# Performance work log

Hardware: AMD Instinct MI355X
Metric: run time of the kernel (lower is better)

## Reference

```python
import jax, jax.numpy as jnp
import numpy as np

N = 50000      # nodes
E = 800000     # edges
F_IN = 128     # in_channels
H = 128        # hidden_channels
C = 10         # num_classes
G = 512        # graphs in batch
EPS = 1e-5     # batchnorm eps


def setup_inputs() -> dict:
    key = jax.random.key(0)
    ks = jax.random.split(key, 18)
    s = 0.05
    return {
        "x": jax.random.normal(ks[0], (N, F_IN), jnp.float32),
        "edge_index": jax.random.randint(ks[1], (2, E), 0, N, dtype=jnp.int32),
        "batch": jnp.sort(jax.random.randint(ks[2], (N,), 0, G, dtype=jnp.int32)),
        "W1": jax.random.normal(ks[3], (F_IN, H), jnp.float32) * s,
        "b1": jnp.zeros((H,), jnp.float32),
        "gamma1": jnp.ones((H,), jnp.float32),
        "beta1": jnp.zeros((H,), jnp.float32),
        "mean1": jax.random.normal(ks[4], (H,), jnp.float32) * 0.1,
        "var1": jax.random.uniform(ks[5], (H,), jnp.float32, 0.5, 1.5),
        "W2": jax.random.normal(ks[6], (H, H), jnp.float32) * s,
        "b2": jnp.zeros((H,), jnp.float32),
        "gamma2": jnp.ones((H,), jnp.float32),
        "beta2": jnp.zeros((H,), jnp.float32),
        "mean2": jax.random.normal(ks[7], (H,), jnp.float32) * 0.1,
        "var2": jax.random.uniform(ks[8], (H,), jnp.float32, 0.5, 1.5),
        "Wlin": jax.random.normal(ks[9], (H, C), jnp.float32) * s,
        "blin": jnp.zeros((C,), jnp.float32),
    }


def _gcn_conv(x, W, b, src, dst):
    # GCNConv with add_self_loops=True, symmetric normalization.
    h = x @ W                                             # [N, H]
    deg = jax.ops.segment_sum(jnp.ones((E,), h.dtype), dst, num_segments=N) + 1.0
    dis = jax.lax.rsqrt(deg)                              # deg^{-1/2}, [N]
    norm = dis[src] * dis[dst]                            # [E]
    agg = jax.ops.segment_sum(h[src] * norm[:, None], dst, num_segments=N)
    agg = agg + h * (dis * dis)[:, None]                  # self-loop term
    return agg + b


def _bn_eval(x, gamma, beta, mean, var):
    return gamma * (x - mean) * jax.lax.rsqrt(var + EPS) + beta


def reference(x, edge_index, batch, W1, b1, gamma1, beta1, mean1, var1,
              W2, b2, gamma2, beta2, mean2, var2, Wlin, blin):
    src, dst = edge_index[0], edge_index[1]
    h = _gcn_conv(x, W1, b1, src, dst)
    h = jax.nn.relu(_bn_eval(h, gamma1, beta1, mean1, var1))
    # dropout: identity in eval mode
    h = _gcn_conv(h, W2, b2, src, dst)
    h = jax.nn.relu(_bn_eval(h, gamma2, beta2, mean2, var2))
    # global_mean_pool over graph ids
    sums = jax.ops.segment_sum(h, batch, num_segments=G)          # [G, H]
    cnts = jax.ops.segment_sum(jnp.ones((N,), h.dtype), batch, num_segments=G)
    pooled = sums / jnp.maximum(cnts, 1.0)[:, None]
    return pooled @ Wlin + blin                                   # [G, C]
```

## Files before the change

kernel.cpp:

```cpp
#include <hip/hip_runtime.h>
#include <hip/hip_bf16.h>
#include <hip/hip_fp16.h>

#define N_NODES 50000
#define N_EDGES 800000
#define HDIM 128
#define NGRAPH 512
#define NCLS 10
#define BN_EPS 1e-5f
#define MAXDEG 64

typedef unsigned int   uint32;
typedef unsigned short u16;
typedef __attribute__((ext_vector_type(8))) _Float16 half8;
typedef __attribute__((ext_vector_type(4))) float f32x4;

__device__ inline u16 f2h(float f) {
    return __half_as_ushort(__float2half(f));
}
__device__ inline float2 h2f2(uint32 u) {
    __half2 h = *(__half2*)&u;
    return __half22float2(h);
}
__device__ inline uint32 packh2(float lo, float hi) {
    return (uint32)f2h(lo) | ((uint32)f2h(hi) << 16);
}

#define GEMM1_BLOCKS 1563
#define W2T_BLOCKS 8
#define FRONT_GRID (W2T_BLOCKS + 3 * GEMM1_BLOCKS)

__global__ __launch_bounds__(256) void front(const float* __restrict__ x,
                                             const float* __restrict__ W1,
                                             u16* __restrict__ bufA,
                                             const int* __restrict__ src,
                                             const int* __restrict__ dst,
                                             int* __restrict__ deg,
                                             u16* __restrict__ epad,
                                             const float* __restrict__ W2,
                                             u16* __restrict__ W2t)
{
    __shared__ float xs[32][36];
    __shared__ float ws[32][128];
    const int tid = threadIdx.x;
    int bid = blockIdx.x;

    if (bid < W2T_BLOCKS) {
        int t0 = bid * 256 + tid;
        for (int i = t0; i < HDIM * HDIM; i += W2T_BLOCKS * 256) {
            int k = i >> 7, n = i & 127;
            W2t[n * HDIM + k] = f2h(W2[i]);
        }
        return;
    }
    bid -= W2T_BLOCKS;
    const int grp = bid / 3, rem = bid % 3;

    if (rem != 0) {
        int e = (grp * 2 + (rem - 1)) * 256 + tid;
        if (e < N_EDGES) {
            int d   = dst[e];
            int pos = atomicAdd(&deg[d], 1);
            epad[d * MAXDEG + pos] = (u16)src[e];
        }
        return;
    }

    const int row0 = grp * 32;
    const int tx   = tid & 31;
    const int ty   = tid >> 5;

    float acc[4][4];
    #pragma unroll
    for (int i = 0; i < 4; ++i)
        #pragma unroll
        for (int j = 0; j < 4; ++j) acc[i][j] = 0.f;

    const int lr = tid >> 3;
    const int lk = (tid & 7) << 2;
    const int wr = tid >> 5;
    const int wc = (tid & 31) << 2;

    for (int k0 = 0; k0 < 128; k0 += 32) {
        float4 xv = make_float4(0.f, 0.f, 0.f, 0.f);
        int grow = row0 + lr;
        if (grow < N_NODES) xv = *(const float4*)(x + (size_t)grow * HDIM + k0 + lk);
        xs[lr][lk] = xv.x; xs[lr][lk + 1] = xv.y; xs[lr][lk + 2] = xv.z; xs[lr][lk + 3] = xv.w;
        #pragma unroll
        for (int i = 0; i < 4; ++i) {
            int kk = wr + i * 8;
            *(float4*)&ws[kk][wc] = *(const float4*)(W1 + (size_t)(k0 + kk) * HDIM + wc);
        }
        __syncthreads();
        #pragma unroll
        for (int kk = 0; kk < 32; kk += 4) {
            float4 wv[4];
            #pragma unroll
            for (int j = 0; j < 4; ++j) wv[j] = *(const float4*)&ws[kk + j][tx << 2];
            #pragma unroll
            for (int i = 0; i < 4; ++i) {
                float4 xr = *(const float4*)&xs[ty * 4 + i][kk];
                acc[i][0] += xr.x * wv[0].x; acc[i][1] += xr.x * wv[0].y;
                acc[i][2] += xr.x * wv[0].z; acc[i][3] += xr.x * wv[0].w;
                acc[i][0] += xr.y * wv[1].x; acc[i][1] += xr.y * wv[1].y;
                acc[i][2] += xr.y * wv[1].z; acc[i][3] += xr.y * wv[1].w;
                acc[i][0] += xr.z * wv[2].x; acc[i][1] += xr.z * wv[2].y;
                acc[i][2] += xr.z * wv[2].z; acc[i][3] += xr.z * wv[2].w;
                acc[i][0] += xr.w * wv[3].x; acc[i][1] += xr.w * wv[3].y;
                acc[i][2] += xr.w * wv[3].z; acc[i][3] += xr.w * wv[3].w;
            }
        }
        __syncthreads();
    }
    #pragma unroll
    for (int i = 0; i < 4; ++i) {
        int grow = row0 + ty * 4 + i;
        if (grow < N_NODES) {
            uint2 o;
            o.x = packh2(acc[i][0], acc[i][1]);
            o.y = packh2(acc[i][2], acc[i][3]);
            *(uint2*)(bufA + (size_t)grow * HDIM + (tx << 2)) = o;
        }
    }
}

#define BT_STRIDE 144
__global__ __launch_bounds__(256) void gemm2_mfma(const u16* __restrict__ A,
                                                  const u16* __restrict__ W2t,
                                                  u16* __restrict__ Y, int nrows)
{
    __shared__ u16 bt[HDIM * BT_STRIDE];
    const int tid = threadIdx.x;
    for (int i = tid; i < HDIM * HDIM / 8; i += 256) {
        int n  = i >> 4;
        int k8 = (i & 15) << 3;
        *(uint4*)&bt[n * BT_STRIDE + k8] = *(const uint4*)&W2t[n * HDIM + k8];
    }
    __syncthreads();

    const int wave = tid >> 6, lane = tid & 63;
    const int rowbase = blockIdx.x * 64 + wave * 16;
    if (rowbase >= nrows) return;
    const int n = lane & 15, q = lane >> 4;

    half8 a[4];
    const u16* arow = A + (size_t)(rowbase + n) * HDIM;
    #pragma unroll
    for (int kc = 0; kc < 4; ++kc)
        a[kc] = *(const half8*)(arow + kc * 32 + q * 8);

    #pragma unroll
    for (int t = 0; t < 8; ++t) {
        f32x4 acc = {0.f, 0.f, 0.f, 0.f};
        #pragma unroll
        for (int kc = 0; kc < 4; ++kc) {
            half8 b = *(const half8*)&bt[(t * 16 + n) * BT_STRIDE + kc * 32 + q * 8];
            acc = __builtin_amdgcn_mfma_f32_16x16x32_f16(a[kc], b, acc, 0, 0, 0);
        }
        #pragma unroll
        for (int r = 0; r < 4; ++r) {
            int grow = rowbase + q * 4 + r;
            Y[(size_t)grow * HDIM + t * 16 + n] = f2h(acc[r]);
        }
    }
}

__global__ __launch_bounds__(256) void gather_bn_relu(const u16* __restrict__ h,
                                                      const u16* __restrict__ epad,
                                                      const int* __restrict__ deg,
                                                      const float* __restrict__ b,
                                                      const float* __restrict__ gamma,
                                                      const float* __restrict__ beta,
                                                      const float* __restrict__ mean,
                                                      const float* __restrict__ var,
                                                      u16* __restrict__ out, int n)
{
    int node = blockIdx.x * 4 + (threadIdx.x >> 6);
    if (node >= n) return;
    const int lane = threadIdx.x & 63;
    const int q    = lane >> 4;
    const int ci   = (lane & 15) << 3;
    const int cnt_e = deg[node];
    const float dd  = rsqrtf((float)cnt_e + 1.0f);

    uint4 hv = *(const uint4*)(h + (size_t)node * HDIM + ci);

    int   s_all  = 0;
    float nm_all = 0.f;
    if (lane < cnt_e) {
        s_all  = epad[node * MAXDEG + lane];
        nm_all = rsqrtf((float)deg[s_all] + 1.0f) * dd;
    }

    float acc[8] = {0.f, 0.f, 0.f, 0.f, 0.f, 0.f, 0.f, 0.f};
    int j = q;
    for (; j + 4 < cnt_e; j += 8) {
        int   s0 = __shfl(s_all, j);     float nm0 = __shfl(nm_all, j);
        int   s1 = __shfl(s_all, j + 4); float nm1 = __shfl(nm_all, j + 4);
        uint4 v0 = *(const uint4*)(h + (size_t)s0 * HDIM + ci);
        uint4 v1 = *(const uint4*)(h + (size_t)s1 * HDIM + ci);
        float2 f0 = h2f2(v0.x), f1 = h2f2(v0.y), f2 = h2f2(v0.z), f3 = h2f2(v0.w);
        acc[0] += f0.x * nm0; acc[1] += f0.y * nm0;
        acc[2] += f1.x * nm0; acc[3] += f1.y * nm0;
        acc[4] += f2.x * nm0; acc[5] += f2.y * nm0;
        acc[6] += f3.x * nm0; acc[7] += f3.y * nm0;
        float2 g0 = h2f2(v1.x), g1 = h2f2(v1.y), g2 = h2f2(v1.z), g3 = h2f2(v1.w);
        acc[0] += g0.x * nm1; acc[1] += g0.y * nm1;
        acc[2] += g1.x * nm1; acc[3] += g1.y * nm1;
        acc[4] += g2.x * nm1; acc[5] += g2.y * nm1;
        acc[6] += g3.x * nm1; acc[7] += g3.y * nm1;
    }
    if (j < cnt_e) {
        int   s0 = __shfl(s_all, j); float nm0 = __shfl(nm_all, j);
        uint4 v0 = *(const uint4*)(h + (size_t)s0 * HDIM + ci);
        float2 f0 = h2f2(v0.x), f1 = h2f2(v0.y), f2 = h2f2(v0.z), f3 = h2f2(v0.w);
        acc[0] += f0.x * nm0; acc[1] += f0.y * nm0;
        acc[2] += f1.x * nm0; acc[3] += f1.y * nm0;
        acc[4] += f2.x * nm0; acc[5] += f2.y * nm0;
        acc[6] += f3.x * nm0; acc[7] += f3.y * nm0;
    }
    #pragma unroll
    for (int k = 0; k < 8; ++k) {
        acc[k] += __shfl_xor(acc[k], 16);
        acc[k] += __shfl_xor(acc[k], 32);
    }

    if (q == 0) {
        float2 g0 = h2f2(hv.x), g1 = h2f2(hv.y), g2 = h2f2(hv.z), g3 = h2f2(hv.w);
        float dd2 = dd * dd;
        float a[8] = {acc[0] + g0.x * dd2, acc[1] + g0.y * dd2,
                      acc[2] + g1.x * dd2, acc[3] + g1.y * dd2,
                      acc[4] + g2.x * dd2, acc[5] + g2.y * dd2,
                      acc[6] + g3.x * dd2, acc[7] + g3.y * dd2};
        float o[8];
        #pragma unroll
        for (int k = 0; k < 8; ++k) {
            int c = ci + k;
            float sc = gamma[c] * rsqrtf(var[c] + BN_EPS);
            float r  = (a[k] + b[c] - mean[c]) * sc + beta[c];
            o[k] = fmaxf(r, 0.f);
        }
        uint4 ov;
        ov.x = packh2(o[0], o[1]); ov.y = packh2(o[2], o[3]);
        ov.z = packh2(o[4], o[5]); ov.w = packh2(o[6], o[7]);
        *(uint4*)(out + (size_t)node * HDIM + ci) = ov;
    }
}

__global__ __launch_bounds__(128) void pool_sum(const u16* __restrict__ h,
                                                const int* __restrict__ batch,
                                                float* __restrict__ sums,
                                                float* __restrict__ cnt, int n)
{
    int c  = threadIdx.x;
    int n0 = blockIdx.x * 32;
    if (n0 >= n) return;
    int nend = min(n0 + 32, n);
    int curg = batch[n0];
    float acc = 0.f;
    int run = 0;
    for (int i = n0; i < nend; ++i) {
        int g   = batch[i];
        float v = __half2float(__ushort_as_half(h[(size_t)i * HDIM + c]));
        if (g != curg) {
            atomicAdd(&sums[(size_t)curg * HDIM + c], acc);
            if (c == 0) atomicAdd(&cnt[curg], (float)run);
            acc = 0.f; run = 0; curg = g;
        }
        acc += v; run++;
    }
    atomicAdd(&sums[(size_t)curg * HDIM + c], acc);
    if (c == 0) atomicAdd(&cnt[curg], (float)run);
}

__global__ __launch_bounds__(128) void final_lin(const float* __restrict__ sums,
                                                 const float* __restrict__ cnt,
                                                 const float* __restrict__ Wlin,
                                                 const float* __restrict__ blin,
                                                 float* __restrict__ out)
{
    __shared__ float red[NCLS][2];
    int g = blockIdx.x;
    int t = threadIdx.x;
    float ic = 1.f / fmaxf(cnt[g], 1.f);
    float v  = sums[(size_t)g * HDIM + t] * ic;
    float p[NCLS];
    #pragma unroll
    for (int c = 0; c < NCLS; ++c) p[c] = v * Wlin[t * NCLS + c];
    #pragma unroll
    for (int c = 0; c < NCLS; ++c) {
        float x = p[c];
        for (int off = 32; off > 0; off >>= 1) x += __shfl_down(x, off);
        if ((t & 63) == 0) red[c][t >> 6] = x;
    }
    __syncthreads();
    if (t < NCLS) out[g * NCLS + t] = red[t][0] + red[t][1] + blin[t];
}

extern "C" void kernel_launch(void* const* d_in, const int* in_sizes, int n_in,
                              void* d_out, int out_size, void* d_ws, size_t ws_size,
                              hipStream_t stream)
{
    const float* x     = (const float*)d_in[0];
    const int*   ei    = (const int*)d_in[1];
    const int*   srcp  = ei;
    const int*   dstp  = ei + N_EDGES;
    const int*   batch = (const int*)d_in[2];
    const float* W1    = (const float*)d_in[3];
    const float* b1    = (const float*)d_in[4];
    const float* g1    = (const float*)d_in[5];
    const float* be1   = (const float*)d_in[6];
    const float* m1    = (const float*)d_in[7];
    const float* v1    = (const float*)d_in[8];
    const float* W2    = (const float*)d_in[9];
    const float* b2    = (const float*)d_in[10];
    const float* g2    = (const float*)d_in[11];
    const float* be2   = (const float*)d_in[12];
    const float* m2    = (const float*)d_in[13];
    const float* v2    = (const float*)d_in[14];
    const float* Wlin  = (const float*)d_in[15];
    const float* blin  = (const float*)d_in[16];
    float*       out   = (float*)d_out;

    int*   deg  = (int*)d_ws;
    float* cnt  = (float*)(deg + N_NODES);
    float* sums = cnt + NGRAPH;
    u16*   bufA = (u16*)(sums + (size_t)NGRAPH * HDIM);
    u16*   bufB = bufA + (size_t)N_NODES * HDIM;
    u16*   epad = bufB + (size_t)N_NODES * HDIM;
    u16*   W2t  = epad + (size_t)N_NODES * MAXDEG;

    hipMemsetAsync(deg, 0,
                   (N_NODES + NGRAPH + (size_t)NGRAPH * HDIM) * sizeof(float), stream);

    front<<<FRONT_GRID, 256, 0, stream>>>(x, W1, bufA, srcp, dstp, deg, epad, W2, W2t);

    const int gather_blocks = (N_NODES + 3) / 4;

    gather_bn_relu<<<gather_blocks, 256, 0, stream>>>(bufA, epad, deg,
                                                      b1, g1, be1, m1, v1, bufB, N_NODES);
    gemm2_mfma<<<(N_NODES + 63) / 64, 256, 0, stream>>>(bufB, W2t, bufA, N_NODES);
    gather_bn_relu<<<gather_blocks, 256, 0, stream>>>(bufA, epad, deg,
                                                      b2, g2, be2, m2, v2, bufB, N_NODES);
    pool_sum<<<(N_NODES + 31) / 32, 128, 0, stream>>>(bufB, batch, sums, cnt, N_NODES);
    final_lin<<<NGRAPH, 128, 0, stream>>>(sums, cnt, Wlin, blin, out);
}
```

Measured before the change: 258.2 us.

## Compute first GCN GEMM with split-fp16 MFMA instead of fp32 SIMT

Replaces the fp32 shared-memory SIMT GEMM for x@W1 in the front kernel with MFMA 16x16x32 f16 instructions. Both x and W1 are split into hi and lo fp16 parts and combined with three MFMAs, to keep accuracy close to fp32. Each GEMM block now covers 64 rows, so the fused front grid is regrouped to four edge-bucketing blocks per GEMM block. Every block converts and transposes the full W1 into LDS using scalar stores, which adds per-block setup cost and may cause bank conflicts.

```diff
diff --git a/kernel.cpp b/kernel.cpp
--- a/kernel.cpp
+++ b/kernel.cpp
@@ -18,6 +18,9 @@
 __device__ inline u16 f2h(float f) {
     return __half_as_ushort(__float2half(f));
 }
+__device__ inline float h2f(u16 u) {
+    return __half2float(__ushort_as_half(u));
+}
 __device__ inline float2 h2f2(uint32 u) {
     __half2 h = *(__half2*)&u;
     return __half22float2(h);
@@ -26,9 +29,10 @@
     return (uint32)f2h(lo) | ((uint32)f2h(hi) << 16);
 }
 
-#define GEMM1_BLOCKS 1563
 #define W2T_BLOCKS 8
-#define FRONT_GRID (W2T_BLOCKS + 3 * GEMM1_BLOCKS)
+#define G1_BLOCKS 782
+#define FRONT_GRID (W2T_BLOCKS + 5 * G1_BLOCKS)
+#define BT_STRIDE 144
 
 __global__ __launch_bounds__(256) void front(const float* __restrict__ x,
                                              const float* __restrict__ W1,
@@ -40,8 +44,8 @@
                                              const float* __restrict__ W2,
                                              u16* __restrict__ W2t)
 {
-    __shared__ float xs[32][36];
-    __shared__ float ws[32][128];
+    __shared__ u16 bt_hi[HDIM * BT_STRIDE];
+    __shared__ u16 bt_lo[HDIM * BT_STRIDE];
     const int tid = threadIdx.x;
     int bid = blockIdx.x;
 
@@ -54,10 +58,10 @@
         return;
     }
     bid -= W2T_BLOCKS;
-    const int grp = bid / 3, rem = bid % 3;
+    const int grp = bid / 5, rem = bid % 5;
 
     if (rem != 0) {
-        int e = (grp * 2 + (rem - 1)) * 256 + tid;
+        int e = (grp * 4 + (rem - 1)) * 256 + tid;
         if (e < N_EDGES) {
             int d   = dst[e];
             int pos = atomicAdd(&deg[d], 1);
@@ -66,65 +70,63 @@
         return;
     }
 
-    const int row0 = grp * 32;
-    const int tx   = tid & 31;
-    const int ty   = tid >> 5;
-
-    float acc[4][4];
-    #pragma unroll
-    for (int i = 0; i < 4; ++i)
-        #pragma unroll
-        for (int j = 0; j < 4; ++j) acc[i][j] = 0.f;
-
-    const int lr = tid >> 3;
-    const int lk = (tid & 7) << 2;
-    const int wr = tid >> 5;
-    const int wc = (tid & 31) << 2;
-
-    for (int k0 = 0; k0 < 128; k0 += 32) {
-        float4 xv = make_float4(0.f, 0.f, 0.f, 0.f);
-        int grow = row0 + lr;
-        if (grow < N_NODES) xv = *(const float4*)(x + (size_t)grow * HDIM + k0 + lk);
-        xs[lr][lk] = xv.x; xs[lr][lk + 1] = xv.y; xs[lr][lk + 2] = xv.z; xs[lr][lk + 3] = xv.w;
-        #pragma unroll
-        for (int i = 0; i < 4; ++i) {
-            int kk = wr + i * 8;
-            *(float4*)&ws[kk][wc] = *(const float4*)(W1 + (size_t)(k0 + kk) * HDIM + wc);
-        }
-        __syncthreads();
-        #pragma unroll
-        for (int kk = 0; kk < 32; kk += 4) {
-            float4 wv[4];
-            #pragma unroll
-            for (int j = 0; j < 4; ++j) wv[j] = *(const float4*)&ws[kk + j][tx << 2];
-            #pragma unroll
-            for (int i = 0; i < 4; ++i) {
-                float4 xr = *(const float4*)&xs[ty * 4 + i][kk];
-                acc[i][0] += xr.x * wv[0].x; acc[i][1] += xr.x * wv[0].y;
-                acc[i][2] += xr.x * wv[0].z; acc[i][3] += xr.x * wv[0].w;
-                acc[i][0] += xr.y * wv[1].x; acc[i][1] += xr.y * wv[1].y;
-                acc[i][2] += xr.y * wv[1].z; acc[i][3] += xr.y * wv[1].w;
-                acc[i][0] += xr.z * wv[2].x; acc[i][1] += xr.z * wv[2].y;
-                acc[i][2] += xr.z * wv[2].z; acc[i][3] += xr.z * wv[2].w;
-                acc[i][0] += xr.w * wv[3].x; acc[i][1] += xr.w * wv[3].y;
-                acc[i][2] += xr.w * wv[3].z; acc[i][3] += xr.w * wv[3].w;
-            }
-        }
-        __syncthreads();
-    }
-    #pragma unroll
-    for (int i = 0; i < 4; ++i) {
-        int grow = row0 + ty * 4 + i;
-        if (grow < N_NODES) {
-            uint2 o;
-            o.x = packh2(acc[i][0], acc[i][1]);
-            o.y = packh2(acc[i][2], acc[i][3]);
-            *(uint2*)(bufA + (size_t)grow * HDIM + (tx << 2)) = o;
-        }
-    }
-}
-
-#define BT_STRIDE 144
+    for (int ii = tid; ii < HDIM * HDIM / 4; ii += 256) {
+        int i = ii << 2;
+        float4 w = *(const float4*)(W1 + i);
+        int k = i >> 7, nn = i & 127;
+        u16 h0 = f2h(w.x), h1 = f2h(w.y), h2 = f2h(w.z), h3 = f2h(w.w);
+        bt_hi[(nn + 0) * BT_STRIDE + k] = h0;
+        bt_hi[(nn + 1) * BT_STRIDE + k] = h1;
+        bt_hi[(nn + 2) * BT_STRIDE + k] = h2;
+        bt_hi[(nn + 3) * BT_STRIDE + k] = h3;
+        bt_lo[(nn + 0) * BT_STRIDE + k] = f2h(w.x - h2f(h0));
+        bt_lo[(nn + 1) * BT_STRIDE + k] = f2h(w.y - h2f(h1));
+        bt_lo[(nn + 2) * BT_STRIDE + k] = f2h(w.z - h2f(h2));
+        bt_lo[(nn + 3) * BT_STRIDE + k] = f2h(w.w - h2f(h3));
+    }
+    __syncthreads();
+
+    const int wave = tid >> 6, lane = tid & 63;
+    const int rowbase = grp * 64 + wave * 16;
+    if (rowbase >= N_NODES) return;
+    const int n = lane & 15, q = lane >> 4;
+
+    half8 a_hi[4], a_lo[4];
+    const float* arow = x + (size_t)(rowbase + n) * HDIM;
+    #pragma unroll
+    for (int kc = 0; kc < 4; ++kc) {
+        float4 lo4 = *(const float4*)(arow + kc * 32 + q * 8);
+        float4 hi4 = *(const float4*)(arow + kc * 32 + q * 8 + 4);
+        float f[8] = {lo4.x, lo4.y, lo4.z, lo4.w, hi4.x, hi4.y, hi4.z, hi4.w};
+        half8 ah, al;
+        #pragma unroll
+        for (int e = 0; e < 8; ++e) {
+            _Float16 h = (_Float16)f[e];
+            ah[e] = h;
+            al[e] = (_Float16)(f[e] - (float)h);
+        }
+        a_hi[kc] = ah; a_lo[kc] = al;
+    }
+
+    #pragma unroll
+    for (int t = 0; t < 8; ++t) {
+        f32x4 acc = {0.f, 0.f, 0.f, 0.f};
+        #pragma unroll
+        for (int kc = 0; kc < 4; ++kc) {
+            half8 bh = *(const half8*)&bt_hi[(t * 16 + n) * BT_STRIDE + kc * 32 + q * 8];
+            half8 bl = *(const half8*)&bt_lo[(t * 16 + n) * BT_STRIDE + kc * 32 + q * 8];
+            acc = __builtin_amdgcn_mfma_f32_16x16x32_f16(a_hi[kc], bh, acc, 0, 0, 0);
+            acc = __builtin_amdgcn_mfma_f32_16x16x32_f16(a_lo[kc], bh, acc, 0, 0, 0);
+            acc = __builtin_amdgcn_mfma_f32_16x16x32_f16(a_hi[kc], bl, acc, 0, 0, 0);
+        }
+        #pragma unroll
+        for (int r = 0; r < 4; ++r) {
+            int grow = rowbase + q * 4 + r;
+            bufA[(size_t)grow * HDIM + t * 16 + n] = f2h(acc[r]);
+        }
+    }
+}
+
 __global__ __launch_bounds__(256) void gemm2_mfma(const u16* __restrict__ A,
                                                   const u16* __restrict__ W2t,
                                                   u16* __restrict__ Y, int nrows)
```

Result: slower. 282.4 us (+9.4%).
